# Optimization experiments

Measured on AMD Instinct MI355X. Metric: run time of the kernel, lower is better.

## Reference

```python
import jax, jax.numpy as jnp
import numpy as np

N_ITER = 50  # bisection iterations (matches entmax_bisect default)


def entmax_bisect(x, alpha):
    """alpha-entmax via bisection along axis=1. x: [B, L, 1], alpha: [1] (>1)."""
    a_m1 = alpha - 1.0
    inv = 1.0 / a_m1
    xs = x * a_m1
    d = x.shape[1]
    max_val = jnp.max(xs, axis=1, keepdims=True)
    tau_lo = max_val - 1.0
    tau_hi = max_val - (1.0 / d) ** a_m1
    f_lo = jnp.sum(jnp.maximum(xs - tau_lo, 0.0) ** inv, axis=1, keepdims=True) - 1.0

    def body(i, carry):
        tau_lo, dm = carry
        dm = dm * 0.5
        tau_m = tau_lo + dm
        f_m = jnp.sum(jnp.maximum(xs - tau_m, 0.0) ** inv, axis=1, keepdims=True) - 1.0
        tau_lo = jnp.where(f_m * f_lo >= 0.0, tau_m, tau_lo)
        return (tau_lo, dm)

    tau_lo, dm = jax.lax.fori_loop(0, N_ITER, body, (tau_lo, tau_hi - tau_lo))
    p = jnp.maximum(xs - (tau_lo + 0.5 * dm), 0.0) ** inv
    return p / jnp.sum(p, axis=1, keepdims=True)


def setup_inputs() -> dict:
    key = jax.random.key(0)
    ks = jax.random.split(key, 8)
    B, L, E2, D = 256, 512, 512, 256  # E2 = emb_size * 2
    C_target = jax.random.normal(ks[0], (B, E2), jnp.float32)
    C = jax.random.normal(ks[1], (B, L, E2), jnp.float32)
    X = jax.random.normal(ks[2], (B, E2, D), jnp.float32)
    alpha = jnp.array([1.5], jnp.float32)  # entmax-1.5
    mask = jax.random.randint(ks[3], (B, L), 0, 2, jnp.int32).at[:, 0].set(1)
    s = 1.0 / np.sqrt(E2)
    Wg1 = jax.random.uniform(ks[4], (E2, E2), jnp.float32, -s, s)
    Wg2 = jax.random.uniform(ks[5], (E2, E2), jnp.float32, -s, s)
    Wg0 = jax.random.uniform(ks[6], (E2, 1), jnp.float32, -s, s)
    bias_alpha = jax.random.normal(ks[7], (E2,), jnp.float32) * 0.02
    return dict(C_target=C_target, C=C, X=X, alpha=alpha, mask=mask,
                Wg1=Wg1, Wg2=Wg2, Wg0=Wg0, bias_alpha=bias_alpha)


def reference(C_target, C, X, alpha, mask, Wg1, Wg2, Wg0, bias_alpha):
    q = C_target[:, None, :]                               # [B, 1, 2E]
    h = jax.nn.relu(C @ Wg1 + q @ Wg2 + bias_alpha)        # [B, L, 2E]
    score = h @ Wg0                                        # [B, L, 1]
    score = jnp.where(mask[..., None] == 0, -1e30, score)  # mask -> -inf
    p = entmax_bisect(score, alpha)                        # sparse attn over L
    attn = jnp.swapaxes(p, 1, 2) @ C                       # [B, 1, 2E]
    out = jnp.sum(attn @ X, axis=1)                        # [B, D]
    return out
```

## Files before the change

### kernel.cpp

```cpp
#include <hip/hip_runtime.h>
#include <hip/hip_bf16.h>

typedef __bf16 bf16_t;
typedef bf16_t bf16x8 __attribute__((ext_vector_type(8)));
typedef float f32x4 __attribute__((ext_vector_type(4)));

__global__ void k_wg1t(const float* __restrict__ Wg1, bf16_t* __restrict__ Wg1T) {
    __shared__ float tile[32][33];
    const int k0 = blockIdx.x * 32;
    const int e0 = blockIdx.y * 32;
    const int tx = threadIdx.x;
    const int ty = threadIdx.y;
    #pragma unroll
    for (int i = 0; i < 32; i += 8)
        tile[ty + i][tx] = Wg1[(k0 + ty + i) * 512 + e0 + tx];
    __syncthreads();
    #pragma unroll
    for (int i = 0; i < 32; i += 8)
        Wg1T[(e0 + ty + i) * 512 + k0 + tx] = (bf16_t)tile[tx][ty + i];
}

__global__ __launch_bounds__(256) void k_gate(const float* __restrict__ Ct,
                                              const float* __restrict__ Wg2,
                                              const float* __restrict__ bias,
                                              float* __restrict__ g) {
    __shared__ float q[512];
    const int b = blockIdx.x;
    const int t = threadIdx.x;
    q[t]       = Ct[b * 512 + t];
    q[t + 256] = Ct[b * 512 + t + 256];
    __syncthreads();
    const int e = (blockIdx.y << 8) + t;
    float acc = bias[e];
    #pragma unroll 8
    for (int k = 0; k < 512; ++k)
        acc = fmaf(q[k], Wg2[k * 512 + e], acc);
    g[b * 512 + e] = acc;
}

__global__ __launch_bounds__(64) void k_compact(const int* __restrict__ mask,
                                                int* __restrict__ idx,
                                                int* __restrict__ nnz) {
    const int b    = blockIdx.x;
    const int lane = threadIdx.x;
    int base = 0;
    #pragma unroll
    for (int c = 0; c < 8; ++c) {
        const int l = (c << 6) + lane;
        const int v = mask[(b << 9) + l];
        const unsigned long long m = __ballot(v != 0);
        const int rank = __popcll(m & ((1ull << lane) - 1ull));
        if (v) idx[(b << 9) + base + rank] = l;
        base += __popcll(m);
    }
    if (lane == 0) nnz[b] = base;
}

__global__ __launch_bounds__(256, 3) void k_score(const float* __restrict__ C,
                                                  const bf16_t* __restrict__ Wg1T,
                                                  const float* __restrict__ g,
                                                  const float* __restrict__ Wg0,
                                                  const int* __restrict__ idx,
                                                  const int* __restrict__ nnz,
                                                  float* __restrict__ score) {
    __shared__ bf16_t As[64 * 32];
    __shared__ bf16_t Bs[256 * 32];
    __shared__ float  sred[4][64];
    __shared__ int    rs[64];

    const int t    = threadIdx.x;
    const int lane = t & 63;
    const int wave = t >> 6;
    const int quad = lane >> 4;
    const int l15  = lane & 15;

    const int bid  = blockIdx.x;
    const int nh   = bid & 1;
    const int tl   = bid >> 1;
    const int b    = tl >> 3;
    const int tile = tl & 7;
    const int nb   = nnz[b];
    if (tile * 64 >= nb) return;

    if (t < 64) {
        const int j = tile * 64 + t;
        rs[t] = idx[(b << 9) + (j < nb ? j : nb - 1)];
    }
    __syncthreads();

    const int r0 = t >> 3,        c0 = (t & 7) << 2;
    const int r1 = 32 + (t >> 3);
    const float* Cb  = C + ((size_t)b << 18);
    const float* pa0 = Cb + (size_t)rs[r0] * 512 + c0;
    const float* pa1 = Cb + (size_t)rs[r1] * 512 + c0;

    float4 va0 = *reinterpret_cast<const float4*>(pa0);
    float4 va1 = *reinterpret_cast<const float4*>(pa1);

    const int ncol0 = nh << 8;
    f32x4 acc[4][4] = {};

    for (int kc = 0; kc < 512; kc += 32) {
        __syncthreads();
        #pragma unroll
        for (int i = 0; i < 4; ++i) {
            const int f  = i * 256 + t;
            const int r  = f >> 2;
            const int c8 = (f & 3) << 3;
            __builtin_amdgcn_global_load_lds(
                (const __attribute__((address_space(1))) void*)(Wg1T + (size_t)(ncol0 + r) * 512 + kc + c8),
                (__attribute__((address_space(3))) void*)(Bs + f * 8), 16, 0, 0);
        }
        {
            union { bf16_t h[4]; uint2 u; } pk;
            pk.h[0] = (bf16_t)va0.x; pk.h[1] = (bf16_t)va0.y;
            pk.h[2] = (bf16_t)va0.z; pk.h[3] = (bf16_t)va0.w;
            *reinterpret_cast<uint2*>(&As[r0 * 32 + c0]) = pk.u;
            pk.h[0] = (bf16_t)va1.x; pk.h[1] = (bf16_t)va1.y;
            pk.h[2] = (bf16_t)va1.z; pk.h[3] = (bf16_t)va1.w;
            *reinterpret_cast<uint2*>(&As[r1 * 32 + c0]) = pk.u;
        }
        if (kc + 32 < 512) {
            va0 = *reinterpret_cast<const float4*>(pa0 + kc + 32);
            va1 = *reinterpret_cast<const float4*>(pa1 + kc + 32);
        }
        __syncthreads();
        bf16x8 afr[4], bfr[4];
        #pragma unroll
        for (int mi = 0; mi < 4; ++mi)
            afr[mi] = *reinterpret_cast<const bf16x8*>(
                &As[(mi * 16 + l15) * 32 + quad * 8]);
        #pragma unroll
        for (int ni = 0; ni < 4; ++ni)
            bfr[ni] = *reinterpret_cast<const bf16x8*>(
                &Bs[(wave * 64 + ni * 16 + l15) * 32 + quad * 8]);
        #pragma unroll
        for (int mi = 0; mi < 4; ++mi)
            #pragma unroll
            for (int ni = 0; ni < 4; ++ni)
                acc[mi][ni] = __builtin_amdgcn_mfma_f32_16x16x32_bf16(
                    afr[mi], bfr[ni], acc[mi][ni], 0, 0, 0);
    }

    float rsum[16];
    #pragma unroll
    for (int i = 0; i < 16; ++i) rsum[i] = 0.f;
    #pragma unroll
    for (int ni = 0; ni < 4; ++ni) {
        const int n  = ncol0 + wave * 64 + ni * 16 + l15;
        const float gv = g[(b << 9) + n];
        const float w0 = Wg0[n];
        #pragma unroll
        for (int mi = 0; mi < 4; ++mi)
            #pragma unroll
            for (int r = 0; r < 4; ++r) {
                const float u = fmaxf(acc[mi][ni][r] + gv, 0.f);
                rsum[mi * 4 + r] = fmaf(u, w0, rsum[mi * 4 + r]);
            }
    }
    #pragma unroll
    for (int i = 0; i < 16; ++i) {
        float v = rsum[i];
        v += __shfl_xor(v, 1);
        v += __shfl_xor(v, 2);
        v += __shfl_xor(v, 4);
        v += __shfl_xor(v, 8);
        rsum[i] = v;
    }
    if (l15 == 0) {
        #pragma unroll
        for (int mi = 0; mi < 4; ++mi)
            #pragma unroll
            for (int r = 0; r < 4; ++r)
                sred[wave][mi * 16 + quad * 4 + r] = rsum[mi * 4 + r];
    }
    __syncthreads();
    if (t < 64) {
        const float sc = sred[0][t] + sred[1][t] + sred[2][t] + sred[3][t];
        if (tile * 64 + t < nb)
            atomicAdd(&score[(b << 9) + rs[t]], sc);
    }
}

__global__ __launch_bounds__(64) void k_entmax(const float* __restrict__ score,
                                               const int* __restrict__ mask,
                                               const float* __restrict__ alpha,
                                               int* __restrict__ sidx,
                                               float* __restrict__ sval,
                                               int* __restrict__ snnz) {
    const int lane = threadIdx.x;
    const int b    = blockIdx.x;
    const float am1 = alpha[0] - 1.0f;
    const float inv = 1.0f / am1;
    const bool  sq  = fabsf(inv - 2.0f) < 1e-6f;
    const float neg = -1e30f * am1;

    const float* sb = score + (b << 9);
    const int*   mb = mask  + (b << 9);
    float x[8];
    {
        const float4 v0 = *reinterpret_cast<const float4*>(sb + lane * 8);
        const float4 v1 = *reinterpret_cast<const float4*>(sb + lane * 8 + 4);
        const int4   m0 = *reinterpret_cast<const int4*>(mb + lane * 8);
        const int4   m1 = *reinterpret_cast<const int4*>(mb + lane * 8 + 4);
        x[0] = m0.x ? v0.x * am1 : neg; x[1] = m0.y ? v0.y * am1 : neg;
        x[2] = m0.z ? v0.z * am1 : neg; x[3] = m0.w ? v0.w * am1 : neg;
        x[4] = m1.x ? v1.x * am1 : neg; x[5] = m1.y ? v1.y * am1 : neg;
        x[6] = m1.z ? v1.z * am1 : neg; x[7] = m1.w ? v1.w * am1 : neg;
    }
    float m = x[0];
    #pragma unroll
    for (int j = 1; j < 8; ++j) m = fmaxf(m, x[j]);
    #pragma unroll
    for (int s = 1; s < 64; s <<= 1) m = fmaxf(m, __shfl_xor(m, s));

    float tau_lo = m - 1.0f;
    float dm = (m - powf(1.0f / 512.0f, am1)) - tau_lo;

    float f_lo;
    {
        float s = 0.f;
        #pragma unroll
        for (int j = 0; j < 8; ++j) {
            const float u = fmaxf(x[j] - tau_lo, 0.f);
            s += sq ? u * u : powf(u, inv);
        }
        #pragma unroll
        for (int sh = 1; sh < 64; sh <<= 1) s += __shfl_xor(s, sh);
        f_lo = s - 1.0f;
    }
    for (int it = 0; it < 50; ++it) {
        dm *= 0.5f;
        const float tau_m = tau_lo + dm;
        float s = 0.f;
        #pragma unroll
        for (int j = 0; j < 8; ++j) {
            const float u = fmaxf(x[j] - tau_m, 0.f);
            s += sq ? u * u : powf(u, inv);
        }
        #pragma unroll
        for (int sh = 1; sh < 64; sh <<= 1) s += __shfl_xor(s, sh);
        if ((s - 1.0f) * f_lo >= 0.f) tau_lo = tau_m;
    }
    const float tau = tau_lo + 0.5f * dm;
    float pj[8];
    float Z = 0.f;
    #pragma unroll
    for (int j = 0; j < 8; ++j) {
        const float u = fmaxf(x[j] - tau, 0.f);
        pj[j] = sq ? u * u : powf(u, inv);
        Z += pj[j];
    }
    #pragma unroll
    for (int sh = 1; sh < 64; sh <<= 1) Z += __shfl_xor(Z, sh);
    const float rz = 1.0f / Z;

    int base = 0;
    #pragma unroll
    for (int j = 0; j < 8; ++j) {
        const float pv = pj[j] * rz;
        const unsigned long long bm = __ballot(pv > 0.f);
        const int rank = __popcll(bm & ((1ull << lane) - 1ull));
        if (pv > 0.f) {
            sidx[(b << 9) + base + rank] = lane * 8 + j;
            sval[(b << 9) + base + rank] = pv;
        }
        base += __popcll(bm);
    }
    if (lane == 0) snnz[b] = base;
}

__global__ __launch_bounds__(256) void k_attn(const int* __restrict__ sidx,
                                              const float* __restrict__ sval,
                                              const int* __restrict__ snnz,
                                              const float* __restrict__ C,
                                              float* __restrict__ attn) {
    __shared__ int   li[512];
    __shared__ float lv[512];
    const int b = blockIdx.x;
    const int t = threadIdx.x;
    const int e = (blockIdx.y << 8) + t;
    const int n = snnz[b];
    for (int i = t; i < n; i += 256) {
        li[i] = sidx[(b << 9) + i];
        lv[i] = sval[(b << 9) + i];
    }
    __syncthreads();
    const float* Cb = C + ((size_t)b << 18);
    float a = 0.f;
    int j = 0;
    for (; j + 8 <= n; j += 8) {
        #pragma unroll
        for (int u = 0; u < 8; ++u)
            a = fmaf(lv[j + u], Cb[((size_t)li[j + u] << 9) + e], a);
    }
    for (; j < n; ++j)
        a = fmaf(lv[j], Cb[((size_t)li[j] << 9) + e], a);
    attn[(b << 9) + e] = a;
}

__global__ __launch_bounds__(256) void k_out(const float* __restrict__ attn,
                                             const float* __restrict__ X,
                                             float* __restrict__ out) {
    __shared__ float as_[128];
    const int b  = blockIdx.x;
    const int ec = blockIdx.y;
    const int t  = threadIdx.x;
    if (t < 128) as_[t] = attn[(b << 9) + (ec << 7) + t];
    __syncthreads();
    const float* Xb = X + (size_t)b * 512 * 256 + (size_t)(ec << 7) * 256;
    float acc = 0.f;
    #pragma unroll 8
    for (int e = 0; e < 128; ++e)
        acc = fmaf(as_[e], Xb[e * 256 + t], acc);
    atomicAdd(&out[(b << 8) + t], acc);
}

extern "C" void kernel_launch(void* const* d_in, const int* in_sizes, int n_in,
                              void* d_out, int out_size, void* d_ws, size_t ws_size,
                              hipStream_t stream) {
    const float* C_target = (const float*)d_in[0];
    const float* C        = (const float*)d_in[1];
    const float* X        = (const float*)d_in[2];
    const float* alpha    = (const float*)d_in[3];
    const int*   mask     = (const int*)  d_in[4];
    const float* Wg1      = (const float*)d_in[5];
    const float* Wg2      = (const float*)d_in[6];
    const float* Wg0      = (const float*)d_in[7];
    const float* bias     = (const float*)d_in[8];
    float* out = (float*)d_out;

    char* ws = (char*)d_ws;
    bf16_t* wg1t  = (bf16_t*)(ws);
    float*  g     = (float*)(ws + ( 512u << 10));
    float*  score = (float*)(ws + (1024u << 10));
    int*    idx   = (int*)  (ws + (1536u << 10));
    int*    sidx  = (int*)  (ws + (2048u << 10));
    float*  sval  = (float*)(ws + (2560u << 10));
    float*  attn  = (float*)(ws + (3072u << 10));
    int*    nnz   = (int*)  (ws + (3584u << 10));
    int*    snnz  = (int*)  (ws + (3584u << 10) + 4096);

    k_wg1t   <<<dim3(16, 16), dim3(32, 8), 0, stream>>>(Wg1, wg1t);
    k_gate   <<<dim3(256, 2), 256, 0, stream>>>(C_target, Wg2, bias, g);
    k_compact<<<256, 64, 0, stream>>>(mask, idx, nnz);
    hipMemsetAsync(score, 0, 512u << 10, stream);
    k_score  <<<4096, 256, 0, stream>>>(C, wg1t, g, Wg0, idx, nnz, score);
    k_entmax <<<256, 64, 0, stream>>>(score, mask, alpha, sidx, sval, snnz);
    k_attn   <<<dim3(256, 2), 256, 0, stream>>>(sidx, sval, snnz, C, attn);
    hipMemsetAsync(d_out, 0, (size_t)out_size * sizeof(float), stream);
    k_out    <<<dim3(256, 4), 256, 0, stream>>>(attn, X, out);
}
```

Baseline: 611.6 us.

## Restructure score GEMM to full-K LDS A tile, split attn over L chunks, vectorize out

k_score now stages the whole 64x512 gathered C tile in LDS as swizzled bf16 and has each block compute all 512 output columns, reading Wg1T fragments straight from global memory. This drops the two-way N split, the per-K-step LDS double sync and the score atomics/memset, but uses 64KB of LDS and lowers occupancy. k_attn splits the nonzero list into 128-entry chunks across blocks with atomic accumulation, and k_out uses float4 loads with a cross-wave reduction over 256-element chunks. k_gate's unroll factor is also raised.

Result: no change. 619.4 us (+1.3%).

```diff
diff --git a/kernel.cpp b/kernel.cpp
--- a/kernel.cpp
+++ b/kernel.cpp
@@ -32,7 +32,7 @@
     __syncthreads();
     const int e = (blockIdx.y << 8) + t;
     float acc = bias[e];
-    #pragma unroll 8
+    #pragma unroll 16
     for (int k = 0; k < 512; ++k)
         acc = fmaf(q[k], Wg2[k * 512 + e], acc);
     g[b * 512 + e] = acc;
@@ -56,15 +56,14 @@
     if (lane == 0) nnz[b] = base;
 }
 
-__global__ __launch_bounds__(256, 3) void k_score(const float* __restrict__ C,
+__global__ __launch_bounds__(256, 2) void k_score(const float* __restrict__ C,
                                                   const bf16_t* __restrict__ Wg1T,
                                                   const float* __restrict__ g,
                                                   const float* __restrict__ Wg0,
                                                   const int* __restrict__ idx,
                                                   const int* __restrict__ nnz,
                                                   float* __restrict__ score) {
-    __shared__ bf16_t As[64 * 32];
-    __shared__ bf16_t Bs[256 * 32];
+    __shared__ bf16_t As[64 * 512];
     __shared__ float  sred[4][64];
     __shared__ int    rs[64];
 
@@ -75,10 +74,8 @@
     const int l15  = lane & 15;
 
     const int bid  = blockIdx.x;
-    const int nh   = bid & 1;
-    const int tl   = bid >> 1;
-    const int b    = tl >> 3;
-    const int tile = tl & 7;
+    const int b    = bid >> 3;
+    const int tile = bid & 7;
     const int nb   = nnz[b];
     if (tile * 64 >= nb) return;
 
@@ -88,56 +85,46 @@
     }
     __syncthreads();
 
-    const int r0 = t >> 3,        c0 = (t & 7) << 2;
-    const int r1 = 32 + (t >> 3);
-    const float* Cb  = C + ((size_t)b << 18);
-    const float* pa0 = Cb + (size_t)rs[r0] * 512 + c0;
-    const float* pa1 = Cb + (size_t)rs[r1] * 512 + c0;
-
-    float4 va0 = *reinterpret_cast<const float4*>(pa0);
-    float4 va1 = *reinterpret_cast<const float4*>(pa1);
-
-    const int ncol0 = nh << 8;
-    f32x4 acc[4][4] = {};
-
-    for (int kc = 0; kc < 512; kc += 32) {
-        __syncthreads();
-        #pragma unroll
-        for (int i = 0; i < 4; ++i) {
-            const int f  = i * 256 + t;
-            const int r  = f >> 2;
-            const int c8 = (f & 3) << 3;
-            __builtin_amdgcn_global_load_lds(
-                (const __attribute__((address_space(1))) void*)(Wg1T + (size_t)(ncol0 + r) * 512 + kc + c8),
-                (__attribute__((address_space(3))) void*)(Bs + f * 8), 16, 0, 0);
-        }
-        {
-            union { bf16_t h[4]; uint2 u; } pk;
-            pk.h[0] = (bf16_t)va0.x; pk.h[1] = (bf16_t)va0.y;
-            pk.h[2] = (bf16_t)va0.z; pk.h[3] = (bf16_t)va0.w;
-            *reinterpret_cast<uint2*>(&As[r0 * 32 + c0]) = pk.u;
-            pk.h[0] = (bf16_t)va1.x; pk.h[1] = (bf16_t)va1.y;
-            pk.h[2] = (bf16_t)va1.z; pk.h[3] = (bf16_t)va1.w;
-            *reinterpret_cast<uint2*>(&As[r1 * 32 + c0]) = pk.u;
-        }
-        if (kc + 32 < 512) {
-            va0 = *reinterpret_cast<const float4*>(pa0 + kc + 32);
-            va1 = *reinterpret_cast<const float4*>(pa1 + kc + 32);
-        }
-        __syncthreads();
-        bf16x8 afr[4], bfr[4];
-        #pragma unroll
-        for (int mi = 0; mi < 4; ++mi)
+    const float* Cb = C + ((size_t)b << 18);
+    char* Asb = reinterpret_cast<char*>(As);
+    #pragma unroll
+    for (int i = 0; i < 32; ++i) {
+        const int f = i * 256 + t;
+        const int r = f >> 7;
+        const int c = (f & 127) << 3;
+        const float4 v = *reinterpret_cast<const float4*>(
+            Cb + (size_t)rs[r] * 512 + ((f & 127) << 2));
+        union { bf16_t h[4]; uint2 u; } pk;
+        pk.h[0] = (bf16_t)v.x; pk.h[1] = (bf16_t)v.y;
+        pk.h[2] = (bf16_t)v.z; pk.h[3] = (bf16_t)v.w;
+        *reinterpret_cast<uint2*>(Asb + r * 1024 + (c ^ ((r & 7) << 4))) = pk.u;
+    }
+    __syncthreads();
+
+    const bf16_t* bp[8];
+    #pragma unroll
+    for (int ni = 0; ni < 8; ++ni)
+        bp[ni] = Wg1T + ((wave * 128 + ni * 16 + l15) << 9) + (quad << 3);
+
+    const int swz = (l15 & 7) << 4;
+    f32x4 acc[4][8] = {};
+    #pragma unroll
+    for (int kc = 0; kc < 16; ++kc) {
+        bf16x8 afr[4], bfr[8];
+        #pragma unroll
+        for (int ni = 0; ni < 8; ++ni)
+            bfr[ni] = *reinterpret_cast<const bf16x8*>(bp[ni] + (kc << 5));
+        #pragma unroll
+        for (int mi = 0; mi < 4; ++mi) {
+            const int r  = mi * 16 + l15;
+            const int cb = ((kc << 6) + (quad << 4)) ^ swz;
             afr[mi] = *reinterpret_cast<const bf16x8*>(
-                &As[(mi * 16 + l15) * 32 + quad * 8]);
-        #pragma unroll
-        for (int ni = 0; ni < 4; ++ni)
-            bfr[ni] = *reinterpret_cast<const bf16x8*>(
-                &Bs[(wave * 64 + ni * 16 + l15) * 32 + quad * 8]);
+                reinterpret_cast<const char*>(As) + (r << 10) + cb);
+        }
         #pragma unroll
         for (int mi = 0; mi < 4; ++mi)
             #pragma unroll
-            for (int ni = 0; ni < 4; ++ni)
+            for (int ni = 0; ni < 8; ++ni)
                 acc[mi][ni] = __builtin_amdgcn_mfma_f32_16x16x32_bf16(
                     afr[mi], bfr[ni], acc[mi][ni], 0, 0, 0);
     }
@@ -146,8 +133,8 @@
     #pragma unroll
     for (int i = 0; i < 16; ++i) rsum[i] = 0.f;
     #pragma unroll
-    for (int ni = 0; ni < 4; ++ni) {
-        const int n  = ncol0 + wave * 64 + ni * 16 + l15;
+    for (int ni = 0; ni < 8; ++ni) {
+        const int n  = wave * 128 + ni * 16 + l15;
         const float gv = g[(b << 9) + n];
         const float w0 = Wg0[n];
         #pragma unroll
@@ -175,10 +162,9 @@
                 sred[wave][mi * 16 + quad * 4 + r] = rsum[mi * 4 + r];
     }
     __syncthreads();
-    if (t < 64) {
+    if (t < 64 && tile * 64 + t < nb) {
         const float sc = sred[0][t] + sred[1][t] + sred[2][t] + sred[3][t];
-        if (tile * 64 + t < nb)
-            atomicAdd(&score[(b << 9) + rs[t]], sc);
+        score[(b << 9) + rs[t]] = sc;
     }
 }
 
@@ -275,45 +261,74 @@
                                               const int* __restrict__ snnz,
                                               const float* __restrict__ C,
                                               float* __restrict__ attn) {
-    __shared__ int   li[512];
-    __shared__ float lv[512];
-    const int b = blockIdx.x;
-    const int t = threadIdx.x;
-    const int e = (blockIdx.y << 8) + t;
-    const int n = snnz[b];
-    for (int i = t; i < n; i += 256) {
-        li[i] = sidx[(b << 9) + i];
-        lv[i] = sval[(b << 9) + i];
+    __shared__ int   li[128];
+    __shared__ float lv[128];
+    const int b  = blockIdx.x;
+    const int ch = blockIdx.y;
+    const int t  = threadIdx.x;
+    const int n  = snnz[b];
+    const int j0 = ch << 7;
+    if (j0 >= n) return;
+    const int cnt = min(n - j0, 128);
+    if (t < cnt) {
+        li[t] = sidx[(b << 9) + j0 + t];
+        lv[t] = sval[(b << 9) + j0 + t];
     }
     __syncthreads();
     const float* Cb = C + ((size_t)b << 18);
-    float a = 0.f;
+    float a0 = 0.f, a1 = 0.f;
     int j = 0;
-    for (; j + 8 <= n; j += 8) {
-        #pragma unroll
-        for (int u = 0; u < 8; ++u)
-            a = fmaf(lv[j + u], Cb[((size_t)li[j + u] << 9) + e], a);
-    }
-    for (; j < n; ++j)
-        a = fmaf(lv[j], Cb[((size_t)li[j] << 9) + e], a);
-    attn[(b << 9) + e] = a;
+    for (; j + 8 <= cnt; j += 8) {
+        #pragma unroll
+        for (int u = 0; u < 8; ++u) {
+            const float  w  = lv[j + u];
+            const float* cr = Cb + ((size_t)li[j + u] << 9);
+            a0 = fmaf(w, cr[t], a0);
+            a1 = fmaf(w, cr[t + 256], a1);
+        }
+    }
+    for (; j < cnt; ++j) {
+        const float  w  = lv[j];
+        const float* cr = Cb + ((size_t)li[j] << 9);
+        a0 = fmaf(w, cr[t], a0);
+        a1 = fmaf(w, cr[t + 256], a1);
+    }
+    atomicAdd(&attn[(b << 9) + t], a0);
+    atomicAdd(&attn[(b << 9) + t + 256], a1);
 }
 
 __global__ __launch_bounds__(256) void k_out(const float* __restrict__ attn,
                                              const float* __restrict__ X,
                                              float* __restrict__ out) {
-    __shared__ float as_[128];
-    const int b  = blockIdx.x;
-    const int ec = blockIdx.y;
-    const int t  = threadIdx.x;
-    if (t < 128) as_[t] = attn[(b << 9) + (ec << 7) + t];
-    __syncthreads();
-    const float* Xb = X + (size_t)b * 512 * 256 + (size_t)(ec << 7) * 256;
-    float acc = 0.f;
+    __shared__ float as_[256];
+    __shared__ f32x4 red[4][64];
+    const int b    = blockIdx.x;
+    const int ec   = blockIdx.y;
+    const int t    = threadIdx.x;
+    const int wave = t >> 6;
+    const int lane = t & 63;
+    as_[t] = attn[(b << 9) + (ec << 8) + t];
+    __syncthreads();
+    const float4* Xb = reinterpret_cast<const float4*>(
+        X + ((size_t)b << 17) + ((size_t)ec << 16));
+    f32x4 a = {};
     #pragma unroll 8
-    for (int e = 0; e < 128; ++e)
-        acc = fmaf(as_[e], Xb[e * 256 + t], acc);
-    atomicAdd(&out[(b << 8) + t], acc);
+    for (int e = wave; e < 256; e += 4) {
+        const float  w = as_[e];
+        const float4 v = Xb[e * 64 + lane];
+        a[0] = fmaf(w, v.x, a[0]);
+        a[1] = fmaf(w, v.y, a[1]);
+        a[2] = fmaf(w, v.z, a[2]);
+        a[3] = fmaf(w, v.w, a[3]);
+    }
+    red[wave][lane] = a;
+    __syncthreads();
+    if (wave == 0) {
+        const f32x4 s = red[0][lane] + red[1][lane] + red[2][lane] + red[3][lane];
+        #pragma unroll
+        for (int r = 0; r < 4; ++r)
+            atomicAdd(&out[(b << 8) + lane * 4 + r], s[r]);
+    }
 }
 
 extern "C" void kernel_launch(void* const* d_in, const int* in_sizes, int n_in,
@@ -344,10 +359,10 @@
     k_wg1t   <<<dim3(16, 16), dim3(32, 8), 0, stream>>>(Wg1, wg1t);
     k_gate   <<<dim3(256, 2), 256, 0, stream>>>(C_target, Wg2, bias, g);
     k_compact<<<256, 64, 0, stream>>>(mask, idx, nnz);
-    hipMemsetAsync(score, 0, 512u << 10, stream);
-    k_score  <<<4096, 256, 0, stream>>>(C, wg1t, g, Wg0, idx, nnz, score);
+    k_score  <<<2048, 256, 0, stream>>>(C, wg1t, g, Wg0, idx, nnz, score);
     k_entmax <<<256, 64, 0, stream>>>(score, mask, alpha, sidx, sval, snnz);
-    k_attn   <<<dim3(256, 2), 256, 0, stream>>>(sidx, sval, snnz, C, attn);
+    hipMemsetAsync(attn, 0, 512u << 10, stream);
+    k_attn   <<<dim3(256, 4), 256, 0, stream>>>(sidx, sval, snnz, C, attn);
     hipMemsetAsync(d_out, 0, (size_t)out_size * sizeof(float), stream);
-    k_out    <<<dim3(256, 4), 256, 0, stream>>>(attn, X, out);
-}
+    k_out    <<<dim3(256, 2), 256, 0, stream>>>(attn, X, out);
+}
```
